# Optimization experiments

Measured on AMD Instinct MI355X. Metric: run time of the kernel, lower is better.

The kernel has to match this reference:

```python
import jax, jax.numpy as jnp
import numpy as np

EPS = 1e-07
WIN_RAD = 1
WIN_DIAM = 2 * WIN_RAD + 1          # 3
WIN_SIZE = WIN_DIAM ** 2            # 9
BAND = 2 * WIN_DIAM - 1             # 5 (possible |dr|,|dc| <= 2)
NBANDS = BAND * BAND                # 25 distinct (dr,dc) offsets
CENTER = NBANDS // 2                # band index of (dr=0,dc=0)


def _extract_patches(img):
    B, C, H, W = img.shape
    Hp, Wp = H - 2 * WIN_RAD, W - 2 * WIN_RAD
    pats = jnp.stack([img[:, :, dy:dy + Hp, dx:dx + Wp]
                      for dy in range(WIN_DIAM) for dx in range(WIN_DIAM)], axis=2)
    return pats.reshape(B, C, WIN_SIZE, Hp * Wp)


def _quadratic(img):
    # per-pixel quadratic form ((X-mu) Sigma^{-1} (X-mu)^T + 1) / win_size -> (B,P,K,K)
    B, C, H, W = img.shape
    pats = _extract_patches(img)                       # (B,C,K,P)
    mean = pats.mean(axis=2)                           # (B,C,P)
    cov = (jnp.einsum('bikp,bjkp->bpij', pats, pats) / WIN_SIZE
           - jnp.einsum('bip,bjp->bpij', mean, mean))  # (B,P,C,C)
    cov = cov + (EPS / WIN_SIZE) * jnp.eye(C, dtype=img.dtype)
    inv_cov = jnp.linalg.inv(cov)                      # (B,P,C,C)
    diff = (pats - mean[:, :, None, :]).transpose(0, 3, 2, 1)  # (B,P,K,C)
    quad = jnp.einsum('bpkc,bpcd,bpld->bpkl', diff, inv_cov, diff)
    return (quad + 1.0) / WIN_SIZE


def _band_indices(H, W):
    # linear pixel index of each patch member (P,K), plus banded (row, band) scatter targets
    Hp, Wp = H - 2 * WIN_RAD, W - 2 * WIN_RAD
    pix = np.arange(H * W, dtype=np.int32).reshape(H, W)
    idx = np.stack([pix[dy:dy + Hp, dx:dx + Wp]
                    for dy in range(WIN_DIAM) for dx in range(WIN_DIAM)], axis=-1)
    idx = idx.reshape(-1, WIN_SIZE)                    # (P,K)
    row = idx[:, :, None]                              # (P,K,1)
    col = idx[:, None, :]                              # (P,1,K)
    dr = col // W - row // W + (BAND // 2)
    dc = col % W - row % W + (BAND // 2)
    band = dr * BAND + dc                              # (P,K,K), always in [0,25)
    row_b = np.broadcast_to(row, band.shape).reshape(-1)
    return jnp.asarray(row_b), jnp.asarray(band.reshape(-1))


def _band_laplacian(quad, H, W):
    # Assemble L = D - W in banded form (B, HW, 25); duplicate (i,j) contributions summed,
    # exactly matching torch.sparse_coo_tensor coalescing + diagonal row-sum construction.
    row_b, band_b = _band_indices(H, W)

    def assemble(q):  # q: (P,K,K)
        Wb = jnp.zeros((H * W, NBANDS), q.dtype).at[row_b, band_b].add(q.reshape(-1))
        d = Wb.sum(axis=1)                             # D_ii = sum_j W_ij
        return (-Wb).at[:, CENTER].add(d)
    return jax.vmap(assemble)(quad)


def reference(content_img, stylized_img):
    B, C, H, W = content_img.shape
    lap_c = _band_laplacian(_quadratic(content_img), H, W)
    lap_s = _band_laplacian(_quadratic(stylized_img), H, W)
    diff = lap_s - lap_c
    # F.mse_loss over the full (B, HW, HW) Laplacians; entries outside the band are
    # identically zero in both, so only banded entries contribute to the sum.
    denom = jnp.asarray(B, diff.dtype) * jnp.asarray(H * W, diff.dtype) ** 2
    return jnp.sum(diff * diff) / denom


if __name__ == '__main__':
    print(reference(**setup_inputs()))


def setup_inputs() -> dict:
    key = jax.random.key(0)
    k1, k2 = jax.random.split(key)
    B, C, H, W = 4, 3, 256, 256
    return {
        'content_img': jax.random.uniform(k1, (B, C, H, W), dtype=jnp.float32),
        'stylized_img': jax.random.uniform(k2, (B, C, H, W), dtype=jnp.float32),
    }
```

## Files before the change

kernel.cpp:

```cpp
#include <hip/hip_runtime.h>

namespace {

constexpr int H = 256;
constexpr int Wd = 256;
constexpr int TILE = 16;
constexpr float EPS9 = 1e-7f / 9.0f;
constexpr float NINTH = 1.0f / 9.0f;
constexpr int IPITCH = 164;

__global__ __launch_bounds__(256, 4)
void matting_loss_kernel(const float* __restrict__ content,
                         const float* __restrict__ stylized,
                         float* __restrict__ ws)
{
    const int b  = blockIdx.z;
    const int x0 = blockIdx.x * TILE;
    const int y0 = blockIdx.y * TILE;
    const int tid = threadIdx.x;
    const int tx = tid & (TILE - 1);
    const int ty = tid >> 4;

    __shared__ __align__(16) float s_img[20 * IPITCH];
    __shared__ __align__(16) float s_muk[2][18][18][4];
    __shared__ __align__(16) float s_A[2][18][18][6];
    __shared__ float s_red[4];

    const size_t bofs = (size_t)b * 3 * H * Wd;
    const float* img0 = content + bofs;
    const float* img1 = stylized + bofs;

    for (int p = tid; p < 400; p += 256) {
        const int py = p / 20, px = p - py * 20;
        const int gy = min(max(y0 - 2 + py, 0), H - 1);
        const int gx = min(max(x0 - 2 + px, 0), Wd - 1);
        const int gi = gy * Wd + gx;
        float4 v0, v1;
        v0.x = img0[gi]; v0.y = img0[H * Wd + gi]; v0.z = img0[2 * H * Wd + gi]; v0.w = 0.f;
        v1.x = img1[gi]; v1.y = img1[H * Wd + gi]; v1.z = img1[2 * H * Wd + gi]; v1.w = 0.f;
        float* dst = &s_img[py * IPITCH + px * 8];
        *reinterpret_cast<float4*>(dst)     = v0;
        *reinterpret_cast<float4*>(dst + 4) = v1;
    }
    __syncthreads();

    for (int p = tid; p < 324; p += 256) {
        const int cy = p / 18, cx = p - cy * 18;
        const int gy = y0 - 1 + cy, gx = x0 - 1 + cx;
        const bool valid = (gy >= 1) && (gy <= H - 2) && (gx >= 1) && (gx <= Wd - 2);
        const float scale = valid ? NINTH : 0.0f;
        #pragma unroll
        for (int m = 0; m < 2; ++m) {
            float s0=0.f,s1=0.f,s2=0.f,q00=0.f,q01=0.f,q02=0.f,q11=0.f,q12=0.f,q22=0.f;
            #pragma unroll
            for (int wy = 0; wy < 3; ++wy)
                #pragma unroll
                for (int wx = 0; wx < 3; ++wx) {
                    const float4 v = *reinterpret_cast<const float4*>(
                        &s_img[(cy + wy) * IPITCH + (cx + wx) * 8 + m * 4]);
                    s0 += v.x; s1 += v.y; s2 += v.z;
                    q00 += v.x * v.x; q01 += v.x * v.y; q02 += v.x * v.z;
                    q11 += v.y * v.y; q12 += v.y * v.z; q22 += v.z * v.z;
                }
            const float mu0 = s0 * NINTH, mu1 = s1 * NINTH, mu2 = s2 * NINTH;
            const float c00 = q00 * NINTH - mu0 * mu0 + EPS9;
            const float c01 = q01 * NINTH - mu0 * mu1;
            const float c02 = q02 * NINTH - mu0 * mu2;
            const float c11 = q11 * NINTH - mu1 * mu1 + EPS9;
            const float c12 = q12 * NINTH - mu1 * mu2;
            const float c22 = q22 * NINTH - mu2 * mu2 + EPS9;
            const float m00 = c11 * c22 - c12 * c12;
            const float m01 = c02 * c12 - c01 * c22;
            const float m02 = c01 * c12 - c02 * c11;
            const float det = c00 * m00 + c01 * m01 + c02 * m02;
            const float invdet = valid ? (1.0f / det) : 0.0f;
            float4 muk; muk.x = mu0; muk.y = mu1; muk.z = mu2; muk.w = scale;
            *reinterpret_cast<float4*>(&s_muk[m][cy][cx][0]) = muk;
            float* A = &s_A[m][cy][cx][0];
            float2 a0; a0.x = m00 * invdet;                  a0.y = m01 * invdet;
            float2 a1; a1.x = m02 * invdet;                  a1.y = (c00*c22 - c02*c02) * invdet;
            float2 a2; a2.x = (c01*c02 - c00*c12) * invdet;  a2.y = (c00*c11 - c01*c01) * invdet;
            reinterpret_cast<float2*>(A)[0] = a0;
            reinterpret_cast<float2*>(A)[1] = a1;
            reinterpret_cast<float2*>(A)[2] = a2;
        }
    }
    __syncthreads();

    float dd[13];
    #pragma unroll
    for (int q = 0; q < 13; ++q) dd[q] = 0.f;

    #pragma unroll
    for (int m = 0; m < 2; ++m) {
        const float sign = (m == 0) ? -1.0f : 1.0f;
        const float4 Ii = *reinterpret_cast<const float4*>(
            &s_img[(ty + 2) * IPITCH + (tx + 2) * 8 + m * 4]);

        float st[3][3][3];
        float ck[3][3];
        #pragma unroll
        for (int ey = 0; ey < 3; ++ey)
        #pragma unroll
        for (int ex = 0; ex < 3; ++ex) {
            const float4 muk = *reinterpret_cast<const float4*>(&s_muk[m][ty + ey][tx + ex][0]);
            const float* Ap = &s_A[m][ty + ey][tx + ex][0];
            const float2 a0 = reinterpret_cast<const float2*>(Ap)[0];
            const float2 a1 = reinterpret_cast<const float2*>(Ap)[1];
            const float2 a2 = reinterpret_cast<const float2*>(Ap)[2];
            const float u0 = Ii.x - muk.x, u1 = Ii.y - muk.y, u2 = Ii.z - muk.z;
            const float t0 = a0.x*u0 + a0.y*u1 + a1.x*u2;
            const float t1 = a0.y*u0 + a1.y*u1 + a2.x*u2;
            const float t2 = a1.x*u0 + a2.x*u1 + a2.y*u2;
            const float s = muk.w;
            st[ey][ex][0] = s*t0; st[ey][ex][1] = s*t1; st[ey][ex][2] = s*t2;
            ck[ey][ex] = s * (1.0f - (t0*muk.x + t1*muk.y + t2*muk.z));
        }

        #pragma unroll
        for (int by = 2; by <= 4; ++by) {
            float4 Jr[5];
            const float* jrow = &s_img[(ty + by) * IPITCH + tx * 8 + m * 4];
            #pragma unroll
            for (int q = 0; q < 5; ++q) {
                if (by == 2 && q < 2) continue;
                Jr[q] = *reinterpret_cast<const float4*>(jrow + q * 8);
            }
            float Rk[3], R[3][3];
            #pragma unroll
            for (int ex = 0; ex < 3; ++ex) {
                float rk = 0.f, r0 = 0.f, r1 = 0.f, r2 = 0.f;
                #pragma unroll
                for (int ey = 0; ey < 3; ++ey) {
                    if (ey >= by - 2) {
                        rk += ck[ey][ex];
                        r0 += st[ey][ex][0]; r1 += st[ey][ex][1]; r2 += st[ey][ex][2];
                    }
                }
                Rk[ex] = rk; R[ex][0] = r0; R[ex][1] = r1; R[ex][2] = r2;
            }
            #pragma unroll
            for (int bx = 0; bx < 5; ++bx) {
                if (by == 2 && bx < 2) continue;
                float Tk = 0.f, T0 = 0.f, T1 = 0.f, T2 = 0.f;
                #pragma unroll
                for (int ex = 0; ex < 3; ++ex) {
                    if (ex >= bx - 2 && ex <= bx) {
                        Tk += Rk[ex];
                        T0 += R[ex][0]; T1 += R[ex][1]; T2 += R[ex][2];
                    }
                }
                const int idx = (by - 2) * 5 + bx - 2;
                const float4 J = Jr[bx];
                dd[idx] += sign * (Tk + T0 * J.x + T1 * J.y + T2 * J.z);
            }
        }
    }

    float loss = dd[0] * dd[0];
    float loss2 = 0.f;
    #pragma unroll
    for (int q = 1; q < 13; ++q) loss2 += dd[q] * dd[q];
    loss += 2.0f * loss2;

    #pragma unroll
    for (int off = 32; off >= 1; off >>= 1)
        loss += __shfl_down(loss, off, 64);
    if ((tid & 63) == 0) s_red[tid >> 6] = loss;
    __syncthreads();
    if (tid == 0) {
        const int bid = (blockIdx.z * gridDim.y + blockIdx.y) * gridDim.x + blockIdx.x;
        ws[bid] = s_red[0] + s_red[1] + s_red[2] + s_red[3];
    }
}

__global__ __launch_bounds__(256)
void reduce_kernel(const float* __restrict__ ws, float* __restrict__ out,
                   int n, float inv_denom)
{
    __shared__ float s_red[4];
    const int tid = threadIdx.x;
    float acc = 0.f;
    for (int i = tid; i < n; i += 256) acc += ws[i];
    #pragma unroll
    for (int off = 32; off >= 1; off >>= 1)
        acc += __shfl_down(acc, off, 64);
    if ((tid & 63) == 0) s_red[tid >> 6] = acc;
    __syncthreads();
    if (tid == 0)
        out[0] = (s_red[0] + s_red[1] + s_red[2] + s_red[3]) * inv_denom;
}

}

extern "C" void kernel_launch(void* const* d_in, const int* in_sizes, int n_in,
                              void* d_out, int out_size, void* d_ws, size_t ws_size,
                              hipStream_t stream) {
    const float* content  = (const float*)d_in[0];
    const float* stylized = (const float*)d_in[1];
    float* out = (float*)d_out;
    float* ws  = (float*)d_ws;

    const int B = in_sizes[0] / (3 * H * Wd);
    const float inv_denom =
        1.0f / ((float)B * (float)(H * Wd) * (float)(H * Wd));

    dim3 grid(Wd / TILE, H / TILE, B);
    const int nblocks = grid.x * grid.y * grid.z;
    matting_loss_kernel<<<grid, 256, 0, stream>>>(content, stylized, ws);
    reduce_kernel<<<1, 256, 0, stream>>>(ws, out, nblocks, inv_denom);
}
```

Measured before the change: 18.58 us.

## Process two rows per thread with taller tiles and per-image shared buffers

Tiles grow from 16x16 to 16x32, so each thread handles two vertically adjacent pixels and reuses the four rows of window statistics (mu, inverse covariance) they share. Halo overhead per output pixel drops. The per-window stats are now computed one image at a time into a single buffer, with syncs between the two passes, and the interleaved image layout is split into two arrays. The cost is higher register pressure (launch bounds lowered to 2 blocks per SM), half as many blocks, and extra barriers.

```diff
diff --git a/kernel.cpp b/kernel.cpp
--- a/kernel.cpp
+++ b/kernel.cpp
@@ -4,33 +4,35 @@
 
 constexpr int H = 256;
 constexpr int Wd = 256;
-constexpr int TILE = 16;
+constexpr int TW = 16;
+constexpr int TH = 32;
 constexpr float EPS9 = 1e-7f / 9.0f;
 constexpr float NINTH = 1.0f / 9.0f;
-constexpr int IPITCH = 164;
-
-__global__ __launch_bounds__(256, 4)
+constexpr int IP = 21 * 4;
+
+__global__ __launch_bounds__(256, 2)
 void matting_loss_kernel(const float* __restrict__ content,
                          const float* __restrict__ stylized,
                          float* __restrict__ ws)
 {
     const int b  = blockIdx.z;
-    const int x0 = blockIdx.x * TILE;
-    const int y0 = blockIdx.y * TILE;
+    const int x0 = blockIdx.x * TW;
+    const int y0 = blockIdx.y * TH;
     const int tid = threadIdx.x;
-    const int tx = tid & (TILE - 1);
-    const int ty = tid >> 4;
-
-    __shared__ __align__(16) float s_img[20 * IPITCH];
-    __shared__ __align__(16) float s_muk[2][18][18][4];
-    __shared__ __align__(16) float s_A[2][18][18][6];
+    const int tx  = tid & 15;
+    const int typ = tid >> 4;
+
+    __shared__ __align__(16) float s_img0[36 * IP];
+    __shared__ __align__(16) float s_img1[36 * IP];
+    __shared__ __align__(16) float s_muk[34][18][4];
+    __shared__ __align__(16) float s_A[34][18][6];
     __shared__ float s_red[4];
 
     const size_t bofs = (size_t)b * 3 * H * Wd;
     const float* img0 = content + bofs;
     const float* img1 = stylized + bofs;
 
-    for (int p = tid; p < 400; p += 256) {
+    for (int p = tid; p < 720; p += 256) {
         const int py = p / 20, px = p - py * 20;
         const int gy = min(max(y0 - 2 + py, 0), H - 1);
         const int gx = min(max(x0 - 2 + px, 0), Wd - 1);
@@ -38,26 +40,33 @@
         float4 v0, v1;
         v0.x = img0[gi]; v0.y = img0[H * Wd + gi]; v0.z = img0[2 * H * Wd + gi]; v0.w = 0.f;
         v1.x = img1[gi]; v1.y = img1[H * Wd + gi]; v1.z = img1[2 * H * Wd + gi]; v1.w = 0.f;
-        float* dst = &s_img[py * IPITCH + px * 8];
-        *reinterpret_cast<float4*>(dst)     = v0;
-        *reinterpret_cast<float4*>(dst + 4) = v1;
+        *reinterpret_cast<float4*>(&s_img0[py * IP + px * 4]) = v0;
+        *reinterpret_cast<float4*>(&s_img1[py * IP + px * 4]) = v1;
     }
-    __syncthreads();
-
-    for (int p = tid; p < 324; p += 256) {
-        const int cy = p / 18, cx = p - cy * 18;
-        const int gy = y0 - 1 + cy, gx = x0 - 1 + cx;
-        const bool valid = (gy >= 1) && (gy <= H - 2) && (gx >= 1) && (gx <= Wd - 2);
-        const float scale = valid ? NINTH : 0.0f;
-        #pragma unroll
-        for (int m = 0; m < 2; ++m) {
+
+    float ddA[13], ddB[13];
+    #pragma unroll
+    for (int q = 0; q < 13; ++q) { ddA[q] = 0.f; ddB[q] = 0.f; }
+
+    #pragma unroll
+    for (int m = 0; m < 2; ++m) {
+        const float* simg = (m == 0) ? s_img0 : s_img1;
+        const float sign  = (m == 0) ? -1.0f : 1.0f;
+
+        __syncthreads();
+
+        for (int p = tid; p < 612; p += 256) {
+            const int cy = p / 18, cx = p - cy * 18;
+            const int gy = y0 + cy - 1, gx = x0 + cx - 1;
+            const bool valid = (gy >= 1) && (gy <= H - 2) && (gx >= 1) && (gx <= Wd - 2);
+            const float scale = valid ? NINTH : 0.0f;
             float s0=0.f,s1=0.f,s2=0.f,q00=0.f,q01=0.f,q02=0.f,q11=0.f,q12=0.f,q22=0.f;
             #pragma unroll
             for (int wy = 0; wy < 3; ++wy)
                 #pragma unroll
                 for (int wx = 0; wx < 3; ++wx) {
                     const float4 v = *reinterpret_cast<const float4*>(
-                        &s_img[(cy + wy) * IPITCH + (cx + wx) * 8 + m * 4]);
+                        &simg[(cy + wy) * IP + (cx + wx) * 4]);
                     s0 += v.x; s1 += v.y; s2 += v.z;
                     q00 += v.x * v.x; q01 += v.x * v.y; q02 += v.x * v.z;
                     q11 += v.y * v.y; q12 += v.y * v.z; q22 += v.z * v.z;
@@ -75,8 +84,8 @@
             const float det = c00 * m00 + c01 * m01 + c02 * m02;
             const float invdet = valid ? (1.0f / det) : 0.0f;
             float4 muk; muk.x = mu0; muk.y = mu1; muk.z = mu2; muk.w = scale;
-            *reinterpret_cast<float4*>(&s_muk[m][cy][cx][0]) = muk;
-            float* A = &s_A[m][cy][cx][0];
+            *reinterpret_cast<float4*>(&s_muk[cy][cx][0]) = muk;
+            float* A = &s_A[cy][cx][0];
             float2 a0; a0.x = m00 * invdet;                  a0.y = m01 * invdet;
             float2 a1; a1.x = m02 * invdet;                  a1.y = (c00*c22 - c02*c02) * invdet;
             float2 a2; a2.x = (c01*c02 - c00*c12) * invdet;  a2.y = (c00*c11 - c01*c01) * invdet;
@@ -84,84 +93,96 @@
             reinterpret_cast<float2*>(A)[1] = a1;
             reinterpret_cast<float2*>(A)[2] = a2;
         }
-    }
-    __syncthreads();
-
-    float dd[13];
-    #pragma unroll
-    for (int q = 0; q < 13; ++q) dd[q] = 0.f;
-
-    #pragma unroll
-    for (int m = 0; m < 2; ++m) {
-        const float sign = (m == 0) ? -1.0f : 1.0f;
-        const float4 Ii = *reinterpret_cast<const float4*>(
-            &s_img[(ty + 2) * IPITCH + (tx + 2) * 8 + m * 4]);
-
-        float st[3][3][3];
-        float ck[3][3];
+        __syncthreads();
+
+        const int r0 = 2 * typ;
+        float stA[3][3][3], ckA[3][3];
+        float stB[3][3][3], ckB[3][3];
+
+        const float4 IiA = *reinterpret_cast<const float4*>(&simg[(r0 + 2) * IP + (tx + 2) * 4]);
+        const float4 IiB = *reinterpret_cast<const float4*>(&simg[(r0 + 3) * IP + (tx + 2) * 4]);
+
         #pragma unroll
-        for (int ey = 0; ey < 3; ++ey)
+        for (int ey0 = 0; ey0 < 4; ++ey0)
         #pragma unroll
         for (int ex = 0; ex < 3; ++ex) {
-            const float4 muk = *reinterpret_cast<const float4*>(&s_muk[m][ty + ey][tx + ex][0]);
-            const float* Ap = &s_A[m][ty + ey][tx + ex][0];
+            const float4 muk = *reinterpret_cast<const float4*>(&s_muk[r0 + ey0][tx + ex][0]);
+            const float* Ap = &s_A[r0 + ey0][tx + ex][0];
             const float2 a0 = reinterpret_cast<const float2*>(Ap)[0];
             const float2 a1 = reinterpret_cast<const float2*>(Ap)[1];
             const float2 a2 = reinterpret_cast<const float2*>(Ap)[2];
-            const float u0 = Ii.x - muk.x, u1 = Ii.y - muk.y, u2 = Ii.z - muk.z;
-            const float t0 = a0.x*u0 + a0.y*u1 + a1.x*u2;
-            const float t1 = a0.y*u0 + a1.y*u1 + a2.x*u2;
-            const float t2 = a1.x*u0 + a2.x*u1 + a2.y*u2;
             const float s = muk.w;
-            st[ey][ex][0] = s*t0; st[ey][ex][1] = s*t1; st[ey][ex][2] = s*t2;
-            ck[ey][ex] = s * (1.0f - (t0*muk.x + t1*muk.y + t2*muk.z));
+            if (ey0 < 3) {
+                const float u0 = IiA.x - muk.x, u1 = IiA.y - muk.y, u2 = IiA.z - muk.z;
+                const float t0 = a0.x*u0 + a0.y*u1 + a1.x*u2;
+                const float t1 = a0.y*u0 + a1.y*u1 + a2.x*u2;
+                const float t2 = a1.x*u0 + a2.x*u1 + a2.y*u2;
+                stA[ey0][ex][0] = s*t0; stA[ey0][ex][1] = s*t1; stA[ey0][ex][2] = s*t2;
+                ckA[ey0][ex] = s * (1.0f - (t0*muk.x + t1*muk.y + t2*muk.z));
+            }
+            if (ey0 > 0) {
+                const float u0 = IiB.x - muk.x, u1 = IiB.y - muk.y, u2 = IiB.z - muk.z;
+                const float t0 = a0.x*u0 + a0.y*u1 + a1.x*u2;
+                const float t1 = a0.y*u0 + a1.y*u1 + a2.x*u2;
+                const float t2 = a1.x*u0 + a2.x*u1 + a2.y*u2;
+                stB[ey0-1][ex][0] = s*t0; stB[ey0-1][ex][1] = s*t1; stB[ey0-1][ex][2] = s*t2;
+                ckB[ey0-1][ex] = s * (1.0f - (t0*muk.x + t1*muk.y + t2*muk.z));
+            }
+        }
+
+        #define BAND_ROW(ST, CK, DD, BY)                                          \
+        {                                                                         \
+            float Rk[3], R[3][3];                                                 \
+            _Pragma("unroll")                                                     \
+            for (int ex = 0; ex < 3; ++ex) {                                      \
+                float rk = 0.f, rr0 = 0.f, rr1 = 0.f, rr2 = 0.f;                  \
+                _Pragma("unroll")                                                 \
+                for (int ey = 0; ey < 3; ++ey) {                                  \
+                    if (ey >= (BY) - 2) {                                         \
+                        rk  += CK[ey][ex];                                        \
+                        rr0 += ST[ey][ex][0]; rr1 += ST[ey][ex][1];               \
+                        rr2 += ST[ey][ex][2];                                     \
+                    }                                                             \
+                }                                                                 \
+                Rk[ex] = rk; R[ex][0] = rr0; R[ex][1] = rr1; R[ex][2] = rr2;      \
+            }                                                                     \
+            _Pragma("unroll")                                                     \
+            for (int bx = 0; bx < 5; ++bx) {                                      \
+                if ((BY) == 2 && bx < 2) continue;                                \
+                float Tk = 0.f, T0 = 0.f, T1 = 0.f, T2 = 0.f;                     \
+                _Pragma("unroll")                                                 \
+                for (int ex = 0; ex < 3; ++ex) {                                  \
+                    if (ex >= bx - 2 && ex <= bx) {                               \
+                        Tk += Rk[ex];                                             \
+                        T0 += R[ex][0]; T1 += R[ex][1]; T2 += R[ex][2];           \
+                    }                                                             \
+                }                                                                 \
+                const int idx = ((BY) - 2) * 5 + bx - 2;                          \
+                const float4 J = Jr[bx];                                          \
+                DD[idx] += sign * (Tk + T0 * J.x + T1 * J.y + T2 * J.z);          \
+            }                                                                     \
         }
 
         #pragma unroll
-        for (int by = 2; by <= 4; ++by) {
+        for (int jr = 0; jr < 4; ++jr) {
             float4 Jr[5];
-            const float* jrow = &s_img[(ty + by) * IPITCH + tx * 8 + m * 4];
+            const float* jrow = &simg[(r0 + 2 + jr) * IP + tx * 4];
             #pragma unroll
             for (int q = 0; q < 5; ++q) {
-                if (by == 2 && q < 2) continue;
-                Jr[q] = *reinterpret_cast<const float4*>(jrow + q * 8);
+                if (jr == 0 && q < 2) continue;
+                Jr[q] = *reinterpret_cast<const float4*>(jrow + q * 4);
             }
-            float Rk[3], R[3][3];
-            #pragma unroll
-            for (int ex = 0; ex < 3; ++ex) {
-                float rk = 0.f, r0 = 0.f, r1 = 0.f, r2 = 0.f;
-                #pragma unroll
-                for (int ey = 0; ey < 3; ++ey) {
-                    if (ey >= by - 2) {
-                        rk += ck[ey][ex];
-                        r0 += st[ey][ex][0]; r1 += st[ey][ex][1]; r2 += st[ey][ex][2];
-                    }
-                }
-                Rk[ex] = rk; R[ex][0] = r0; R[ex][1] = r1; R[ex][2] = r2;
-            }
-            #pragma unroll
-            for (int bx = 0; bx < 5; ++bx) {
-                if (by == 2 && bx < 2) continue;
-                float Tk = 0.f, T0 = 0.f, T1 = 0.f, T2 = 0.f;
-                #pragma unroll
-                for (int ex = 0; ex < 3; ++ex) {
-                    if (ex >= bx - 2 && ex <= bx) {
-                        Tk += Rk[ex];
-                        T0 += R[ex][0]; T1 += R[ex][1]; T2 += R[ex][2];
-                    }
-                }
-                const int idx = (by - 2) * 5 + bx - 2;
-                const float4 J = Jr[bx];
-                dd[idx] += sign * (Tk + T0 * J.x + T1 * J.y + T2 * J.z);
-            }
-        }
+            if (jr <= 2) BAND_ROW(stA, ckA, ddA, (2 + jr))
+            if (jr >= 1) BAND_ROW(stB, ckB, ddB, (1 + jr))
+        }
+        #undef BAND_ROW
     }
 
-    float loss = dd[0] * dd[0];
+    float loss1 = ddA[0] * ddA[0] + ddB[0] * ddB[0];
     float loss2 = 0.f;
     #pragma unroll
-    for (int q = 1; q < 13; ++q) loss2 += dd[q] * dd[q];
-    loss += 2.0f * loss2;
+    for (int q = 1; q < 13; ++q) loss2 += ddA[q] * ddA[q] + ddB[q] * ddB[q];
+    float loss = loss1 + 2.0f * loss2;
 
     #pragma unroll
     for (int off = 32; off >= 1; off >>= 1)
@@ -205,7 +226,7 @@
     const float inv_denom =
         1.0f / ((float)B * (float)(H * Wd) * (float)(H * Wd));
 
-    dim3 grid(Wd / TILE, H / TILE, B);
+    dim3 grid(Wd / TW, H / TH, B);
     const int nblocks = grid.x * grid.y * grid.z;
     matting_loss_kernel<<<grid, 256, 0, stream>>>(content, stylized, ws);
     reduce_kernel<<<1, 256, 0, stream>>>(ws, out, nblocks, inv_denom);
```

After: 20.90 us. +12.5%, slower.
